# Optimization experiments

Measured on AMD Instinct MI355X. Metric: run time of the kernel, lower is better.

## Reference

```python
import jax, jax.numpy as jnp
import numpy as np

GAMMA = 0.99
ETA = 0.1
PHI = 0.9
EPS_FLOOR_NEWTON = 1e-8
EPS_FLOOR_BETA = 1e-6
N_NEWTON = 20


def _epsilon_cosh(r):
    # r: [B, N] nonnegative residuals; per-row Newton solve for epsilon s.t.
    # mean(sinh(r/eps)) == 1 along axis 1.
    N = r.shape[1]
    r_max = jnp.maximum(jnp.max(r, axis=1, keepdims=True), EPS_FLOOR_NEWTON)
    eps = r_max / (jnp.log(jnp.asarray(2.0 * N, dtype=r.dtype)) + EPS_FLOOR_NEWTON)
    for _ in range(N_NEWTON):
        eps_safe = jnp.maximum(eps, EPS_FLOOR_NEWTON)
        u = r / eps_safe  # [B, N]
        val = jnp.mean(jnp.sinh(u), axis=1, keepdims=True) - 1.0
        grad = jnp.mean(jnp.cosh(u) * (-u / eps_safe), axis=1, keepdims=True)
        eps = eps - val / (grad - EPS_FLOOR_NEWTON)
    return jnp.maximum(eps, EPS_FLOOR_NEWTON)


def _update_spatial_weights(r_i, Lambda, it):
    # 'cosh' weighting potential branch of update_spatial_weights
    del it  # unused by the cosh branch
    eps_q = _epsilon_cosh(r_i)                       # [B, 1]
    beta = 1.0 / (eps_q + EPS_FLOOR_BETA)            # [B, 1]
    q = jnp.sinh(beta * r_i)                         # [B, N]
    q_max = jnp.max(q, axis=1, keepdims=True)
    q_norm = q / (q_max + 1e-20)
    lambda_it = PHI * q_norm + (1.0 - PHI)
    return GAMMA * Lambda + ETA * lambda_it


def setup_inputs() -> dict:
    key = jax.random.key(0)
    k1, k2, k3 = jax.random.split(key, 3)
    B, N = 2048, 8192
    y_pred = jax.random.normal(k1, (B, N), dtype=jnp.float32)
    y_true = jax.random.normal(k2, (B, N), dtype=jnp.float32)
    Lambda = jax.random.uniform(k3, (B, N), dtype=jnp.float32)
    return {"y_pred": y_pred, "y_true": y_true, "Lambda": Lambda, "it": 100}


def reference(y_pred, y_true, Lambda, it):
    r_i = jnp.abs(y_true - y_pred)
    # weights are computed on detached residuals
    updated_Lambda = _update_spatial_weights(jax.lax.stop_gradient(r_i), Lambda, it)
    loss = jnp.mean(jnp.square(updated_Lambda * r_i))
    return (loss, updated_Lambda)
```

## Files before the change

kernel.cpp:

```cpp
#include <hip/hip_runtime.h>
#include <math.h>

#define N_COLS 8192
#define BLOCK  256
#define NW     (BLOCK / 64)
#define VPT    (N_COLS / BLOCK)

__global__ void zero_out_kernel(float* out) {
    if (threadIdx.x == 0 && blockIdx.x == 0) out[0] = 0.0f;
}

__device__ __forceinline__ void block_reduce_sum2(float& a, float& b,
                                                  float2* s_part, int tid) {
    const int lane = tid & 63;
    const int wid  = tid >> 6;
    #pragma unroll
    for (int m = 32; m >= 1; m >>= 1) {
        a += __shfl_xor(a, m, 64);
        b += __shfl_xor(b, m, 64);
    }
    __syncthreads();
    if (lane == 0) s_part[wid] = make_float2(a, b);
    __syncthreads();
    float2 p0 = s_part[0], p1 = s_part[1], p2 = s_part[2], p3 = s_part[3];
    a = (p0.x + p1.x) + (p2.x + p3.x);
    b = (p0.y + p1.y) + (p2.y + p3.y);
}

__device__ __forceinline__ float block_reduce_max(float a, float* s_part, int tid) {
    const int lane = tid & 63;
    const int wid  = tid >> 6;
    #pragma unroll
    for (int m = 32; m >= 1; m >>= 1) {
        a = fmaxf(a, __shfl_xor(a, m, 64));
    }
    __syncthreads();
    if (lane == 0) s_part[wid] = a;
    __syncthreads();
    return fmaxf(fmaxf(s_part[0], s_part[1]), fmaxf(s_part[2], s_part[3]));
}

__global__ __launch_bounds__(BLOCK) void custom_loss_kernel(
        const float* __restrict__ y_pred,
        const float* __restrict__ y_true,
        const float* __restrict__ Lambda,
        float* __restrict__ out,
        float inv_total) {
    __shared__ float2 s_part2[NW];
    __shared__ float  s_part1[NW];

    const int row = blockIdx.x;
    const int tid = threadIdx.x;
    const size_t base = (size_t)row * N_COLS;
    const float* yp = y_pred + base;
    const float* yt = y_true + base;

    float r[VPT];
    float rmax = 0.0f;
    #pragma unroll
    for (int j = 0; j < VPT; ++j) {
        const int idx = j * BLOCK + tid;
        float rv = fabsf(yt[idx] - yp[idx]);
        r[j] = rv;
        rmax = fmaxf(rmax, rv);
    }
    rmax = block_reduce_max(rmax, s_part1, tid);
    rmax = fmaxf(rmax, 1e-8f);

    const float denom = logf(2.0f * (float)N_COLS) + 1e-8f;
    float eps = rmax / denom;

    const float scale = 0.5f / (float)N_COLS;
    for (int it = 0; it < 20; ++it) {
        const float eps_safe = fmaxf(eps, 1e-8f);
        const float inv_eps = 1.0f / eps_safe;
        float s_sinh = 0.0f, s_coshu = 0.0f;
        #pragma unroll
        for (int j = 0; j < VPT; ++j) {
            float u  = r[j] * inv_eps;
            float e  = __expf(u);
            float ei = __expf(-u);
            s_sinh += (e - ei);
            s_coshu = fmaf(e + ei, u, s_coshu);
        }
        block_reduce_sum2(s_sinh, s_coshu, s_part2, tid);
        float val  = fmaf(s_sinh, scale, -1.0f);
        float grad = -(s_coshu * scale) * inv_eps;
        float delta = val / (grad - 1e-8f);
        eps = eps - delta;
        if (fabsf(delta) <= 1e-6f * eps) break;
    }
    eps = fmaxf(eps, 1e-8f);
    const float beta = 1.0f / (eps + 1e-6f);

    float q[VPT];
    float qmax = 0.0f;
    #pragma unroll
    for (int j = 0; j < VPT; ++j) {
        float u  = beta * r[j];
        float e  = __expf(u);
        float ei = __expf(-u);
        float qv = 0.5f * (e - ei);
        q[j] = qv;
        qmax = fmaxf(qmax, qv);
    }
    qmax = block_reduce_max(qmax, s_part1, tid);
    const float inv_qmax = 1.0f / (qmax + 1e-20f);

    const float* lam = Lambda + base;
    float* outw = out + 1 + base;
    float s_loss = 0.0f;
    #pragma unroll
    for (int j = 0; j < VPT; ++j) {
        const int idx = j * BLOCK + tid;
        float L = lam[idx];
        float lam_it = fmaf(0.9f, q[j] * inv_qmax, 0.1f);
        float uL = fmaf(0.99f, L, 0.1f * lam_it);
        outw[idx] = uL;
        float t = uL * r[j];
        s_loss = fmaf(t, t, s_loss);
    }
    float dummy = 0.0f;
    block_reduce_sum2(s_loss, dummy, s_part2, tid);
    if (tid == 0) atomicAdd(out, s_loss * inv_total);
}

extern "C" void kernel_launch(void* const* d_in, const int* in_sizes, int n_in,
                              void* d_out, int out_size, void* d_ws, size_t ws_size,
                              hipStream_t stream) {
    const float* y_pred = (const float*)d_in[0];
    const float* y_true = (const float*)d_in[1];
    const float* Lambda = (const float*)d_in[2];
    float* out = (float*)d_out;

    const int total = in_sizes[0];
    const int B = total / N_COLS;
    const float inv_total = 1.0f / (float)total;

    hipLaunchKernelGGL(zero_out_kernel, dim3(1), dim3(64), 0, stream, out);
    hipLaunchKernelGGL(custom_loss_kernel, dim3(B), dim3(BLOCK), 0, stream,
                       y_pred, y_true, Lambda, out, inv_total);
}
```

Baseline: 226.2 us.

## Solve Newton epsilon on a shared-memory residual histogram instead of full rows

Builds a 1024-bin shared-memory histogram of residuals per row and runs the Newton iterations over bin midpoints with a single wave, instead of evaluating exp over all 8192 residuals per iteration. qmax is computed analytically from rmax, and loads use float4. This removes most transcendental work in the iterative solve. The cost is approximation error in epsilon from binning, plus a looser convergence tolerance.

```diff
diff --git a/kernel.cpp b/kernel.cpp
--- a/kernel.cpp
+++ b/kernel.cpp
@@ -3,41 +3,13 @@
 
 #define N_COLS 8192
 #define BLOCK  256
-#define NW     (BLOCK / 64)
-#define VPT    (N_COLS / BLOCK)
+#define NW     4
+#define F4PT   (N_COLS / BLOCK / 4)
+#define NBINS  1024
+#define BPL    (NBINS / 64)
 
 __global__ void zero_out_kernel(float* out) {
     if (threadIdx.x == 0 && blockIdx.x == 0) out[0] = 0.0f;
-}
-
-__device__ __forceinline__ void block_reduce_sum2(float& a, float& b,
-                                                  float2* s_part, int tid) {
-    const int lane = tid & 63;
-    const int wid  = tid >> 6;
-    #pragma unroll
-    for (int m = 32; m >= 1; m >>= 1) {
-        a += __shfl_xor(a, m, 64);
-        b += __shfl_xor(b, m, 64);
-    }
-    __syncthreads();
-    if (lane == 0) s_part[wid] = make_float2(a, b);
-    __syncthreads();
-    float2 p0 = s_part[0], p1 = s_part[1], p2 = s_part[2], p3 = s_part[3];
-    a = (p0.x + p1.x) + (p2.x + p3.x);
-    b = (p0.y + p1.y) + (p2.y + p3.y);
-}
-
-__device__ __forceinline__ float block_reduce_max(float a, float* s_part, int tid) {
-    const int lane = tid & 63;
-    const int wid  = tid >> 6;
-    #pragma unroll
-    for (int m = 32; m >= 1; m >>= 1) {
-        a = fmaxf(a, __shfl_xor(a, m, 64));
-    }
-    __syncthreads();
-    if (lane == 0) s_part[wid] = a;
-    __syncthreads();
-    return fmaxf(fmaxf(s_part[0], s_part[1]), fmaxf(s_part[2], s_part[3]));
 }
 
 __global__ __launch_bounds__(BLOCK) void custom_loss_kernel(
@@ -46,83 +18,127 @@
         const float* __restrict__ Lambda,
         float* __restrict__ out,
         float inv_total) {
-    __shared__ float2 s_part2[NW];
-    __shared__ float  s_part1[NW];
+    __shared__ unsigned int s_hist[NBINS];
+    __shared__ float s_wmax[NW];
+    __shared__ float s_part[NW];
+    __shared__ float s_bcast[2];
 
-    const int row = blockIdx.x;
-    const int tid = threadIdx.x;
+    const int row  = blockIdx.x;
+    const int tid  = threadIdx.x;
+    const int lane = tid & 63;
+    const int wid  = tid >> 6;
     const size_t base = (size_t)row * N_COLS;
-    const float* yp = y_pred + base;
-    const float* yt = y_true + base;
+    const float4* yp4 = (const float4*)(y_pred + base);
+    const float4* yt4 = (const float4*)(y_true + base);
 
-    float r[VPT];
+    float4 r[F4PT];
     float rmax = 0.0f;
     #pragma unroll
-    for (int j = 0; j < VPT; ++j) {
-        const int idx = j * BLOCK + tid;
-        float rv = fabsf(yt[idx] - yp[idx]);
+    for (int j = 0; j < F4PT; ++j) {
+        const int g = j * BLOCK + tid;
+        float4 a = yt4[g];
+        float4 b = yp4[g];
+        float4 rv;
+        rv.x = fabsf(a.x - b.x); rv.y = fabsf(a.y - b.y);
+        rv.z = fabsf(a.z - b.z); rv.w = fabsf(a.w - b.w);
         r[j] = rv;
-        rmax = fmaxf(rmax, rv);
+        rmax = fmaxf(rmax, fmaxf(fmaxf(rv.x, rv.y), fmaxf(rv.z, rv.w)));
     }
-    rmax = block_reduce_max(rmax, s_part1, tid);
+    #pragma unroll
+    for (int m = 32; m >= 1; m >>= 1) rmax = fmaxf(rmax, __shfl_xor(rmax, m, 64));
+    #pragma unroll
+    for (int i = 0; i < NBINS / BLOCK; ++i) s_hist[tid + i * BLOCK] = 0u;
+    __syncthreads();
+    if (lane == 0) s_wmax[wid] = rmax;
+    __syncthreads();
+    rmax = fmaxf(fmaxf(s_wmax[0], s_wmax[1]), fmaxf(s_wmax[2], s_wmax[3]));
     rmax = fmaxf(rmax, 1e-8f);
 
-    const float denom = logf(2.0f * (float)N_COLS) + 1e-8f;
-    float eps = rmax / denom;
+    const float hscale = (float)NBINS / rmax;
+    #pragma unroll
+    for (int j = 0; j < F4PT; ++j) {
+        unsigned bx = min((unsigned)(r[j].x * hscale), (unsigned)(NBINS - 1));
+        unsigned by = min((unsigned)(r[j].y * hscale), (unsigned)(NBINS - 1));
+        unsigned bz = min((unsigned)(r[j].z * hscale), (unsigned)(NBINS - 1));
+        unsigned bw = min((unsigned)(r[j].w * hscale), (unsigned)(NBINS - 1));
+        atomicAdd(&s_hist[bx], 1u);
+        atomicAdd(&s_hist[by], 1u);
+        atomicAdd(&s_hist[bz], 1u);
+        atomicAdd(&s_hist[bw], 1u);
+    }
+    __syncthreads();
 
-    const float scale = 0.5f / (float)N_COLS;
-    for (int it = 0; it < 20; ++it) {
-        const float eps_safe = fmaxf(eps, 1e-8f);
-        const float inv_eps = 1.0f / eps_safe;
-        float s_sinh = 0.0f, s_coshu = 0.0f;
-        #pragma unroll
-        for (int j = 0; j < VPT; ++j) {
-            float u  = r[j] * inv_eps;
-            float e  = __expf(u);
-            float ei = __expf(-u);
-            s_sinh += (e - ei);
-            s_coshu = fmaf(e + ei, u, s_coshu);
+    if (wid == 0) {
+        float eps = rmax / (logf(2.0f * (float)N_COLS) + 1e-8f);
+        const float binw = rmax * (1.0f / (float)NBINS);
+        const float sc2  = 0.5f / (float)N_COLS;
+        for (int it = 0; it < 20; ++it) {
+            const float inv_eps = 1.0f / fmaxf(eps, 1e-8f);
+            float fs = 0.0f, gs = 0.0f;
+            #pragma unroll
+            for (int k = 0; k < BPL; ++k) {
+                const int b = lane + 64 * k;
+                float n = (float)s_hist[b];
+                float m = ((float)b + 0.5f) * binw;
+                float u = m * inv_eps;
+                float e  = __expf(u);
+                float ei = __expf(-u);
+                fs = fmaf(n, e - ei, fs);
+                gs = fmaf(n * (e + ei), u, gs);
+            }
+            #pragma unroll
+            for (int m2 = 32; m2 >= 1; m2 >>= 1) {
+                fs += __shfl_xor(fs, m2, 64);
+                gs += __shfl_xor(gs, m2, 64);
+            }
+            float val  = fmaf(fs, sc2, -1.0f);
+            float grad = -(gs * sc2) * inv_eps;
+            float delta = val / (grad - 1e-8f);
+            eps -= delta;
+            if (fabsf(delta) <= 1e-5f * eps) break;
         }
-        block_reduce_sum2(s_sinh, s_coshu, s_part2, tid);
-        float val  = fmaf(s_sinh, scale, -1.0f);
-        float grad = -(s_coshu * scale) * inv_eps;
-        float delta = val / (grad - 1e-8f);
-        eps = eps - delta;
-        if (fabsf(delta) <= 1e-6f * eps) break;
+        eps = fmaxf(eps, 1e-8f);
+        const float beta = 1.0f / (eps + 1e-6f);
+        const float um = beta * rmax;
+        const float qmax = 0.5f * (__expf(um) - __expf(-um));
+        if (lane == 0) {
+            s_bcast[0] = beta;
+            s_bcast[1] = 1.0f / (qmax + 1e-20f);
+        }
     }
-    eps = fmaxf(eps, 1e-8f);
-    const float beta = 1.0f / (eps + 1e-6f);
+    __syncthreads();
+    const float beta     = s_bcast[0];
+    const float inv_qmax = s_bcast[1];
 
-    float q[VPT];
-    float qmax = 0.0f;
-    #pragma unroll
-    for (int j = 0; j < VPT; ++j) {
-        float u  = beta * r[j];
-        float e  = __expf(u);
-        float ei = __expf(-u);
-        float qv = 0.5f * (e - ei);
-        q[j] = qv;
-        qmax = fmaxf(qmax, qv);
-    }
-    qmax = block_reduce_max(qmax, s_part1, tid);
-    const float inv_qmax = 1.0f / (qmax + 1e-20f);
-
-    const float* lam = Lambda + base;
+    const float4* lam4 = (const float4*)(Lambda + base);
     float* outw = out + 1 + base;
     float s_loss = 0.0f;
     #pragma unroll
-    for (int j = 0; j < VPT; ++j) {
-        const int idx = j * BLOCK + tid;
-        float L = lam[idx];
-        float lam_it = fmaf(0.9f, q[j] * inv_qmax, 0.1f);
-        float uL = fmaf(0.99f, L, 0.1f * lam_it);
-        outw[idx] = uL;
-        float t = uL * r[j];
-        s_loss = fmaf(t, t, s_loss);
+    for (int j = 0; j < F4PT; ++j) {
+        const int g = j * BLOCK + tid;
+        float4 L = lam4[g];
+        float rr[4] = {r[j].x, r[j].y, r[j].z, r[j].w};
+        float LL[4] = {L.x, L.y, L.z, L.w};
+        #pragma unroll
+        for (int c = 0; c < 4; ++c) {
+            float u  = beta * rr[c];
+            float q  = 0.5f * (__expf(u) - __expf(-u));
+            float lam_it = fmaf(0.9f, q * inv_qmax, 0.1f);
+            float uL = fmaf(0.99f, LL[c], 0.1f * lam_it);
+            outw[(size_t)g * 4 + c] = uL;
+            float t = uL * rr[c];
+            s_loss = fmaf(t, t, s_loss);
+        }
     }
-    float dummy = 0.0f;
-    block_reduce_sum2(s_loss, dummy, s_part2, tid);
-    if (tid == 0) atomicAdd(out, s_loss * inv_total);
+    #pragma unroll
+    for (int m = 32; m >= 1; m >>= 1) s_loss += __shfl_xor(s_loss, m, 64);
+    __syncthreads();
+    if (lane == 0) s_part[wid] = s_loss;
+    __syncthreads();
+    if (tid == 0) {
+        float tot = (s_part[0] + s_part[1]) + (s_part[2] + s_part[3]);
+        atomicAdd(out, tot * inv_total);
+    }
 }
 
 extern "C" void kernel_launch(void* const* d_in, const int* in_sizes, int n_in,
```

New measurement: 226.0 us. No clear change (-0.1%).
